# Kernel optimization log

Measured on AMD Instinct MI355X. Metric: run time of the kernel, lower is better.

## Reference

```python
import jax, jax.numpy as jnp
import numpy as np

# dims: S=seq_len, E=nenv, H=max_human_num, D=human_embedding_size, A=attention_size, NH=heads
S, E, H, D, A, NH = 128, 256, 20, 64, 64, 8
NEG = -1e9


def setup_inputs() -> dict:
    key = jax.random.key(0)
    ks = jax.random.split(key, 9)
    sc = 1.0 / np.sqrt(D).astype(np.float32)
    return {
        "h_temporal": jax.random.normal(ks[0], (S, E, 1, D), jnp.float32),
        "h_spatials": jax.random.normal(ks[1], (S, E, H, D), jnp.float32),
        "each_seq_len": jax.random.randint(ks[2], (S * E,), 0, H, dtype=jnp.int32),
        # per-head Linear params, stored [in, out] (equivalent to torch y = x W^T + b)
        "Wt": jax.random.normal(ks[3], (NH, D, A), jnp.float32) * sc,
        "bt": jax.random.normal(ks[4], (NH, A), jnp.float32) * 0.01,
        "Ws": jax.random.normal(ks[5], (NH, D, A), jnp.float32) * sc,
        "bs": jax.random.normal(ks[6], (NH, A), jnp.float32) * 0.01,
        # final merge linear: concat over heads (NH*D) -> D
        "Wf": jax.random.normal(ks[7], (NH * D, D), jnp.float32) / np.sqrt(NH * D).astype(np.float32),
        "bf": jax.random.normal(ks[8], (D,), jnp.float32) * 0.01,
    }


def reference(h_temporal, h_spatials, each_seq_len, Wt, bt, Ws, bs, Wf, bf):
    s, e, h, d = h_spatials.shape
    a = Wt.shape[-1]
    nh = Wt.shape[0]

    # per-head embeddings (heads vectorized instead of python loop)
    # temporal: [s,e,1,d] -> [s,e,nh,a] (the size-1 edge dim is summed out == squeeze)
    te = jnp.einsum('seoh,nha->sena', h_temporal, Wt) + bt            # [s,e,nh,a]
    sp = jnp.einsum('semh,nha->senma', h_spatials, Ws) + bs[:, None]  # [s,e,nh,h,a]

    # elementwise-product scoring, summed over attention dim, scaled by num_edges/sqrt(A)
    temperature = h / np.sqrt(a).astype(np.float32)
    scores = jnp.einsum('sena,senma->senm', te, sp) * temperature     # [s,e,nh,h]

    # mask: True for neighbor index j < each_seq_len (cumsum-of-onehot trick, closed form)
    mask = (jnp.arange(h)[None, :] < each_seq_len[:, None]).reshape(s, e, h)
    scores = jnp.where(mask[:, :, None, :], scores, NEG)
    attn = jax.nn.softmax(scores, axis=-1)                            # [s,e,nh,h]

    # weighted sum of spatial hidden states (the tiny bmm), per head
    wv = jnp.einsum('senm,semh->senh', attn, h_spatials)              # [s,e,nh,d]

    # concat heads (head-major, matching torch.cat over last dim) + final merge linear
    out = wv.reshape(s, e, 1, nh * d) @ Wf + bf                       # [s,e,1,d]
    return out
```

## Files before the change

### kernel.cpp

```cpp
#include <hip/hip_runtime.h>
#include <hip/hip_bf16.h>

typedef __attribute__((ext_vector_type(8))) short short8;
typedef __attribute__((ext_vector_type(4))) float f32x4;

constexpr float TEMP = 2.5f;
constexpr float NEGV = -1e9f;

constexpr int K_OFF  = 0;
constexpr int P_OFF  = 512;
constexpr int Q_OFF  = 1024;
constexpr int PFRAG  = 1040;
constexpr int MFRAG  = 2064;
constexpr int WFRAG  = 34832;

constexpr int HS2_U   = 0;
constexpr int HS2_PL  = 11520;
constexpr int V2_U    = 23040;
constexpr int V2_PL   = 4672;
constexpr int HT2_U   = 32384;
constexpr int ATT_F = 16832;
constexpr int C_F   = 18752;
constexpr int LEN_F = 18816;
constexpr int LDS_FL = 18824;

#define MFMA_B16 __builtin_amdgcn_mfma_f32_16x16x32_bf16

__device__ inline ushort bf16_rne(float x) {
  uint u = __float_as_uint(x);
  u += 0x7FFF + ((u >> 16) & 1);
  return (ushort)(u >> 16);
}
__device__ inline float bf16_f(ushort h) { return __uint_as_float(((uint)h) << 16); }
__device__ inline void split2(float x, ushort& h0, ushort& h1) {
  h0 = bf16_rne(x);
  h1 = bf16_rne(x - bf16_f(h0));
}
__device__ inline ushort split_lvl2(float x, int s) {
  ushort h0 = bf16_rne(x);
  return s == 0 ? h0 : bf16_rne(x - bf16_f(h0));
}
__device__ inline uint2 pkbf16x4(float4 v) {
  __hip_bfloat162 h0 = __float22bfloat162_rn(make_float2(v.x, v.y));
  __hip_bfloat162 h1 = __float22bfloat162_rn(make_float2(v.z, v.w));
  uint2 r; __builtin_memcpy(&r.x, &h0, 4); __builtin_memcpy(&r.y, &h1, 4);
  return r;
}
__device__ inline void pksplit4(float4 v, uint2& u0, uint2& u1) {
  u0 = pkbf16x4(v);
  float4 r;
  r.x = v.x - __uint_as_float(u0.x << 16);
  r.y = v.y - __uint_as_float(u0.x & 0xffff0000u);
  r.z = v.z - __uint_as_float(u0.y << 16);
  r.w = v.w - __uint_as_float(u0.y & 0xffff0000u);
  u1 = pkbf16x4(r);
}

__global__ __launch_bounds__(256) void prep_kernel(
    const float* __restrict__ Wt, const float* __restrict__ bt,
    const float* __restrict__ Ws, const float* __restrict__ bs,
    const float* __restrict__ Wf, float* __restrict__ ws) {
  __shared__ float AL[64 * 65];
  __shared__ float BL[64 * 65];
  __shared__ float ML[64 * 65];
  const int t = threadIdx.x;
  uint* wsu = (uint*)ws;
  if (blockIdx.x < 8) {
    const int n = blockIdx.x;
#pragma unroll
    for (int i = 0; i < 16; ++i) {
      int idx = i * 256 + t;
      AL[(idx >> 6) * 65 + (idx & 63)] = Wt[n * 4096 + idx];
      BL[(idx >> 6) * 65 + (idx & 63)] = Ws[n * 4096 + idx];
    }
    __syncthreads();
#pragma unroll
    for (int i = 0; i < 16; ++i) {
      int idx = i * 256 + t;
      int dp = idx >> 6, d = idx & 63;
      float acc = 0.f;
#pragma unroll 8
      for (int a = 0; a < 64; ++a) acc += AL[dp * 65 + a] * BL[d * 65 + a];
      ML[dp * 65 + d] = acc * TEMP;
    }
    if (t < 64) {
      float acc = 0.f;
#pragma unroll 8
      for (int a = 0; a < 64; ++a) acc += BL[t * 65 + a] * bt[n * 64 + a];
      ws[K_OFF + n * 64 + t] = acc * TEMP;
    } else if (t < 128) {
      int r = t - 64;
      float acc = 0.f;
#pragma unroll 8
      for (int a = 0; a < 64; ++a) acc += AL[r * 65 + a] * bs[n * 64 + a];
      ws[P_OFF + n * 64 + r] = acc * TEMP;
    } else if (t == 128) {
      float acc = 0.f;
      for (int a = 0; a < 64; ++a) acc += bt[n * 64 + a] * bs[n * 64 + a];
      ws[Q_OFF + n] = acc * TEMP;
    }
    __syncthreads();
#pragma unroll
    for (int i = 0; i < 16; ++i) {
      int f = i * 256 + t;
      int r = f & 3, lane = (f >> 2) & 63, g = f >> 8;
      int s = g & 1, dt = (g >> 1) & 3, ks = g >> 3;
      int k = ks * 32 + ((lane >> 4) & 3) * 8 + r * 2;
      int d = dt * 16 + (lane & 15);
      uint lo = split_lvl2(ML[k * 65 + d], s);
      uint hi = split_lvl2(ML[(k + 1) * 65 + d], s);
      wsu[MFRAG + n * 4096 + (((ks * 4 + dt) * 2 + s) * 64 + lane) * 4 + r] =
          lo | (hi << 16);
    }
  } else if (blockIdx.x < 16) {
    const int n = blockIdx.x - 8;
#pragma unroll
    for (int i = 0; i < 16; ++i) {
      int idx = i * 256 + t;
      AL[(idx >> 6) * 65 + (idx & 63)] = Wf[(n * 64 + (idx >> 6)) * 64 + (idx & 63)];
    }
    __syncthreads();
#pragma unroll
    for (int i = 0; i < 16; ++i) {
      int f = i * 256 + t;
      int r = f & 3, lane = (f >> 2) & 63, g = f >> 8;
      int s = g & 1, dt = (g >> 1) & 3, ks = g >> 3;
      int k = ks * 32 + ((lane >> 4) & 3) * 8 + r * 2;
      int d = dt * 16 + (lane & 15);
      uint lo = split_lvl2(AL[k * 65 + d], s);
      uint hi = split_lvl2(AL[(k + 1) * 65 + d], s);
      wsu[WFRAG + n * 4096 + (((ks * 4 + dt) * 2 + s) * 64 + lane) * 4 + r] =
          lo | (hi << 16);
    }
  } else {
#pragma unroll
    for (int i = 0; i < 2; ++i) {
      int idx = i * 256 + t;
      int n = idx >> 6, dp = idx & 63;
      float acc = 0.f;
#pragma unroll 8
      for (int a = 0; a < 64; ++a)
        acc += Wt[n * 4096 + dp * 64 + a] * bs[n * 64 + a];
      AL[idx] = acc * TEMP;
    }
    __syncthreads();
#pragma unroll
    for (int i = 0; i < 4; ++i) {
      int f = i * 256 + t;
      int r = f & 3, lane = (f >> 2) & 63, g = f >> 8;
      int s = g & 1, ks = g >> 1;
      int k = ks * 32 + ((lane >> 4) & 3) * 8 + r * 2;
      int col = lane & 15;
      uint lo = (col < 8) ? (uint)split_lvl2(AL[col * 64 + k], s) : 0u;
      uint hi = (col < 8) ? (uint)split_lvl2(AL[col * 64 + k + 1], s) : 0u;
      wsu[PFRAG + ((ks * 2 + s) * 64 + lane) * 4 + r] = lo | (hi << 16);
    }
  }
}

#define SPLIT2_MFMA(FB, DT, CC)                                      \
  {                                                                  \
    short8 b00 = *(const short8*)&(FB)[((0 * 4 + (DT)) * 2 + 0) * 256]; \
    short8 b01 = *(const short8*)&(FB)[((0 * 4 + (DT)) * 2 + 1) * 256]; \
    short8 b10 = *(const short8*)&(FB)[((1 * 4 + (DT)) * 2 + 0) * 256]; \
    short8 b11 = *(const short8*)&(FB)[((1 * 4 + (DT)) * 2 + 1) * 256]; \
    CC = MFMA_B16(a00, b00, CC, 0, 0, 0);                            \
    CC = MFMA_B16(a10, b10, CC, 0, 0, 0);                            \
    CC = MFMA_B16(a00, b01, CC, 0, 0, 0);                            \
    CC = MFMA_B16(a01, b00, CC, 0, 0, 0);                            \
    CC = MFMA_B16(a10, b11, CC, 0, 0, 0);                            \
    CC = MFMA_B16(a11, b10, CC, 0, 0, 0);                            \
  }

#define LOAD_A(BASEU, ROWSTR, PLANESTR, ROW, KOFF)                   \
  short8 a00 = *(const short8*)&(BASEU)[(ROW) * (ROWSTR) + (KOFF)];               \
  short8 a01 = *(const short8*)&(BASEU)[(PLANESTR) + (ROW) * (ROWSTR) + (KOFF)];  \
  short8 a10 = *(const short8*)&(BASEU)[(ROW) * (ROWSTR) + 32 + (KOFF)];          \
  short8 a11 = *(const short8*)&(BASEU)[(PLANESTR) + (ROW) * (ROWSTR) + 32 + (KOFF)];

#define HV_LOAD(I, DST)                                                      \
  {                                                                          \
    const int f_ = (I) * 512 + t;                                            \
    const int p_ = f_ / 320;                                                 \
    const int s_ = f_ - p_ * 320;                                            \
    DST = *(const float4*)(hs_g + (size_t)(pair0 + p_) * 1280 +              \
                           (s_ >> 4) * 64 + (s_ & 15) * 4);                  \
  }
#define HV_STORE(I, SRC)                                                     \
  {                                                                          \
    const int f_ = (I) * 512 + t;                                            \
    const int p_ = f_ / 320;                                                 \
    const int s_ = f_ - p_ * 320;                                            \
    uint2 u0_, u1_; pksplit4(SRC, u0_, u1_);                                 \
    ushort* d_ = ldsu + HS2_U + p_ * 1440 + (s_ >> 4) * 72 + (s_ & 15) * 4;  \
    *(uint2*)d_ = u0_;                                                       \
    *(uint2*)(d_ + HS2_PL) = u1_;                                            \
  }

__global__ __launch_bounds__(512, 4) void attn_kernel(
    const float* __restrict__ ht_g, const float* __restrict__ hs_g,
    const int* __restrict__ len_g, const float* __restrict__ bf,
    const float* __restrict__ wsp, float* __restrict__ out) {
  __shared__ __align__(16) float lds[LDS_FL];
  ushort* ldsu = (ushort*)lds;
  const int t    = threadIdx.x;
  const int lane = t & 63;
  const int w    = t >> 6;
  const int pair0 = blockIdx.x * 8;
  const uint* wsu = (const uint*)wsp;

  {
    float x = ht_g[(size_t)pair0 * 64 + t];
    ushort h0, h1; split2(x, h0, h1);
    const int p = t >> 6, dp = t & 63;
    ldsu[HT2_U + 0 * 640 + p * 80 + dp] = h0;
    ldsu[HT2_U + 1 * 640 + p * 80 + dp] = h1;
  }
  if (t < 8) lds[LEN_F + t] = (float)len_g[pair0 + t];
  __syncthreads();

  const int lo4 = lane & 15, kg = lane >> 4;
  const int rp8 = lo4 & 7;

  {
    const int n = w;
    LOAD_A(ldsu + HT2_U, 80, 640, rp8, kg * 8)
    const uint* fb = wsu + MFRAG + n * 4096 + lane * 4;
    const float* kb = &wsp[K_OFF + n * 64 + lo4];
    float kv0 = kb[0], kv1 = kb[16], kv2 = kb[32], kv3 = kb[48];
    f32x4 c0 = {kv0, kv0, kv0, kv0};
    f32x4 c1 = {kv1, kv1, kv1, kv1};
    f32x4 c2 = {kv2, kv2, kv2, kv2};
    f32x4 c3 = {kv3, kv3, kv3, kv3};
    SPLIT2_MFMA(fb, 0, c0)
    SPLIT2_MFMA(fb, 1, c1)
    SPLIT2_MFMA(fb, 2, c2)
    SPLIT2_MFMA(fb, 3, c3)
    if (kg < 2) {
#pragma unroll
      for (int reg = 0; reg < 4; ++reg) {
        const int p = kg * 4 + reg;
        ushort* vp = ldsu + V2_U + p * 584 + n * 72 + lo4;
        ushort h0, h1;
        split2(c0[reg], h0, h1); vp[0]  = h0; vp[V2_PL]      = h1;
        split2(c1[reg], h0, h1); vp[16] = h0; vp[V2_PL + 16] = h1;
        split2(c2[reg], h0, h1); vp[32] = h0; vp[V2_PL + 32] = h1;
        split2(c3[reg], h0, h1); vp[48] = h0; vp[V2_PL + 48] = h1;
      }
    }
  }

  float4 hv0, hv1, hv2, hv3, hv4;
  HV_LOAD(0, hv0) HV_LOAD(1, hv1) HV_LOAD(2, hv2) HV_LOAD(3, hv3) HV_LOAD(4, hv4)

  if (w == 0) {
    LOAD_A(ldsu + HT2_U, 80, 640, rp8, kg * 8)
    const uint* fbp = wsu + PFRAG + lane * 4;
    short8 b00 = *(const short8*)&fbp[0 * 256];
    short8 b01 = *(const short8*)&fbp[1 * 256];
    short8 b10 = *(const short8*)&fbp[2 * 256];
    short8 b11 = *(const short8*)&fbp[3 * 256];
    float qv = (lo4 < 8) ? wsp[Q_OFF + lo4] : 0.f;
    f32x4 cc = {qv, qv, qv, qv};
    cc = MFMA_B16(a00, b00, cc, 0, 0, 0);
    cc = MFMA_B16(a10, b10, cc, 0, 0, 0);
    cc = MFMA_B16(a00, b01, cc, 0, 0, 0);
    cc = MFMA_B16(a01, b00, cc, 0, 0, 0);
    cc = MFMA_B16(a10, b11, cc, 0, 0, 0);
    cc = MFMA_B16(a11, b10, cc, 0, 0, 0);
    if (kg < 2 && lo4 < 8) {
#pragma unroll
      for (int reg = 0; reg < 4; ++reg)
        lds[C_F + (kg * 4 + reg) * 8 + lo4] = cc[reg];
    }
  }

  HV_STORE(0, hv0) HV_STORE(1, hv1) HV_STORE(2, hv2) HV_STORE(3, hv3) HV_STORE(4, hv4)
  __syncthreads();

  {
    const int p = w;
    const int n8 = rp8;
    const int lenp = (int)lds[LEN_F + p];
    const ushort* vb = ldsu + V2_U + p * 584 + n8 * 72;
    const short8 B00 = *(const short8*)&vb[kg * 8];
    const short8 B01 = *(const short8*)&vb[V2_PL + kg * 8];
    const short8 B10 = *(const short8*)&vb[32 + kg * 8];
    const short8 B11 = *(const short8*)&vb[V2_PL + 32 + kg * 8];
    const float cv = lds[C_F + p * 8 + n8];
    f32x4 acc0 = {cv, cv, cv, cv};
    f32x4 acc1 = {cv, cv, cv, cv};
    {
      const ushort* ab = ldsu + HS2_U + p * 1440;
      LOAD_A(ab, 72, HS2_PL, lo4, kg * 8)
      acc0 = MFMA_B16(a00, B00, acc0, 0, 0, 0);
      acc0 = MFMA_B16(a10, B10, acc0, 0, 0, 0);
      acc0 = MFMA_B16(a00, B01, acc0, 0, 0, 0);
      acc0 = MFMA_B16(a01, B00, acc0, 0, 0, 0);
      acc0 = MFMA_B16(a10, B11, acc0, 0, 0, 0);
      acc0 = MFMA_B16(a11, B10, acc0, 0, 0, 0);
    }
    {
      const int row = (16 + lo4 < 20) ? (16 + lo4) : 19;
      const ushort* ab = ldsu + HS2_U + p * 1440;
      LOAD_A(ab, 72, HS2_PL, row, kg * 8)
      acc1 = MFMA_B16(a00, B00, acc1, 0, 0, 0);
      acc1 = MFMA_B16(a10, B10, acc1, 0, 0, 0);
      acc1 = MFMA_B16(a00, B01, acc1, 0, 0, 0);
      acc1 = MFMA_B16(a01, B00, acc1, 0, 0, 0);
      acc1 = MFMA_B16(a10, B11, acc1, 0, 0, 0);
      acc1 = MFMA_B16(a11, B10, acc1, 0, 0, 0);
    }
    float e0[4], e1[4];
    float mx = NEGV;
#pragma unroll
    for (int r = 0; r < 4; ++r) {
      const int m0 = kg * 4 + r;
      const int m1 = 16 + kg * 4 + r;
      e0[r] = (m0 < lenp) ? acc0[r] : NEGV;
      e1[r] = (m1 < lenp) ? acc1[r] : NEGV;
      mx = fmaxf(mx, fmaxf(e0[r], e1[r]));
    }
    mx = fmaxf(mx, __shfl_xor(mx, 16));
    mx = fmaxf(mx, __shfl_xor(mx, 32));
    float sm = 0.f;
#pragma unroll
    for (int r = 0; r < 4; ++r) {
      e0[r] = __expf(e0[r] - mx);
      e1[r] = (kg == 0) ? __expf(e1[r] - mx) : 0.f;
      sm += e0[r] + e1[r];
    }
    sm += __shfl_xor(sm, 16);
    sm += __shfl_xor(sm, 32);
    const float inv = 1.0f / sm;
    if (lo4 < 8) {
#pragma unroll
      for (int r = 0; r < 4; ++r)
        lds[ATT_F + p * 240 + (kg * 4 + r) * 12 + lo4] = e0[r] * inv;
      if (kg == 0) {
#pragma unroll
        for (int r = 0; r < 4; ++r)
          lds[ATT_F + p * 240 + (16 + r) * 12 + lo4] = e1[r] * inv;
      }
    }
  }

  {
    const int p = w, d = lane;
    const ushort* hsb = ldsu + HS2_U + p * 1440;
    float wv[8] = {0.f, 0.f, 0.f, 0.f, 0.f, 0.f, 0.f, 0.f};
    const float* atp = &lds[ATT_F + p * 240];
#pragma unroll
    for (int m_ = 0; m_ < 20; ++m_) {
      const float h = bf16_f(hsb[m_ * 72 + d]);
      const float4 a0 = *(const float4*)&atp[m_ * 12];
      const float4 a1 = *(const float4*)&atp[m_ * 12 + 4];
      wv[0] += a0.x * h; wv[1] += a0.y * h; wv[2] += a0.z * h; wv[3] += a0.w * h;
      wv[4] += a1.x * h; wv[5] += a1.y * h; wv[6] += a1.z * h; wv[7] += a1.w * h;
    }
    ushort* wp = ldsu + V2_U + p * 584;
#pragma unroll
    for (int n = 0; n < 8; ++n) {
      ushort h0, h1; split2(wv[n], h0, h1);
      wp[n * 72 + d] = h0;
      wp[V2_PL + n * 72 + d] = h1;
    }
  }
  __syncthreads();

  {
    const int dt = w & 3, ng = w >> 2;
    f32x4 cc = {0.f, 0.f, 0.f, 0.f};
#pragma unroll
    for (int nn = 0; nn < 4; ++nn) {
      const int n = ng * 4 + nn;
      LOAD_A(ldsu + V2_U, 584, V2_PL, rp8, n * 72 + kg * 8)
      const uint* fb = wsu + WFRAG + n * 4096 + lane * 4;
      SPLIT2_MFMA(fb, dt, cc)
    }
    if (kg < 2) {
#pragma unroll
      for (int reg = 0; reg < 4; ++reg)
        lds[0 + ng * 512 + (kg * 4 + reg) * 64 + dt * 16 + lo4] = cc[reg];
    }
  }
  __syncthreads();

  {
    const int d = t & 63;
    out[(size_t)pair0 * 64 + t] = bf[d] + lds[t] + lds[512 + t];
  }
}

extern "C" void kernel_launch(void* const* d_in, const int* in_sizes, int n_in,
                              void* d_out, int out_size, void* d_ws, size_t ws_size,
                              hipStream_t stream) {
  const float* ht  = (const float*)d_in[0];
  const float* hs  = (const float*)d_in[1];
  const int*   len = (const int*)d_in[2];
  const float* Wt  = (const float*)d_in[3];
  const float* bt  = (const float*)d_in[4];
  const float* Ws  = (const float*)d_in[5];
  const float* bs  = (const float*)d_in[6];
  const float* Wf  = (const float*)d_in[7];
  const float* bf  = (const float*)d_in[8];
  float* outp = (float*)d_out;
  float* ws   = (float*)d_ws;

  hipLaunchKernelGGL(prep_kernel, dim3(17), dim3(256), 0, stream,
                     Wt, bt, Ws, bs, Wf, ws);
  hipLaunchKernelGGL(attn_kernel, dim3(4096), dim3(512), 0, stream,
                     ht, hs, len, bf, ws, outp);
}
```

Baseline: 94.50 us.

## Use MFMA for attention-weighted sum and single-bf16 Wf with preloaded fragments

Replaces the scalar FMA loop for the per-head weighted sum of spatial states with bf16 MFMA ops, rounding attention weights to bf16. Drops the two-level bf16 split of Wf to a single bf16 plane, halving its workspace footprint and MFMA count in the merge stage. The Wf fragments are also loaded into registers at kernel start so their latency overlaps the earlier stages. This reduces precision in two places and raises register pressure, which may affect occupancy.

```diff
diff --git a/kernel.cpp b/kernel.cpp
--- a/kernel.cpp
+++ b/kernel.cpp
@@ -54,6 +54,11 @@
   r.z = v.z - __uint_as_float(u0.y << 16);
   r.w = v.w - __uint_as_float(u0.y & 0xffff0000u);
   u1 = pkbf16x4(r);
+}
+__device__ inline short8 pack4(uint a, uint b, uint c, uint d) {
+  union { uint u[4]; short8 s; } cv;
+  cv.u[0] = a; cv.u[1] = b; cv.u[2] = c; cv.u[3] = d;
+  return cv.s;
 }
 
 __global__ __launch_bounds__(256) void prep_kernel(
@@ -121,15 +126,15 @@
     }
     __syncthreads();
 #pragma unroll
-    for (int i = 0; i < 16; ++i) {
+    for (int i = 0; i < 8; ++i) {
       int f = i * 256 + t;
       int r = f & 3, lane = (f >> 2) & 63, g = f >> 8;
-      int s = g & 1, dt = (g >> 1) & 3, ks = g >> 3;
+      int dt = g & 3, ks = g >> 2;
       int k = ks * 32 + ((lane >> 4) & 3) * 8 + r * 2;
       int d = dt * 16 + (lane & 15);
-      uint lo = split_lvl2(AL[k * 65 + d], s);
-      uint hi = split_lvl2(AL[(k + 1) * 65 + d], s);
-      wsu[WFRAG + n * 4096 + (((ks * 4 + dt) * 2 + s) * 64 + lane) * 4 + r] =
+      uint lo = bf16_rne(AL[k * 65 + d]);
+      uint hi = bf16_rne(AL[(k + 1) * 65 + d]);
+      wsu[WFRAG + n * 2048 + ((ks * 4 + dt) * 64 + lane) * 4 + r] =
           lo | (hi << 16);
     }
   } else {
@@ -208,6 +213,17 @@
   const int w    = t >> 6;
   const int pair0 = blockIdx.x * 8;
   const uint* wsu = (const uint*)wsp;
+  const int lo4 = lane & 15, kg = lane >> 4;
+  const int rp8 = lo4 & 7;
+  const int dtw = w & 3, ngw = w >> 2;
+
+  short8 wfB0[4], wfB1[4];
+#pragma unroll
+  for (int nn = 0; nn < 4; ++nn) {
+    const uint* fb = wsu + WFRAG + (ngw * 4 + nn) * 2048 + lane * 4;
+    wfB0[nn] = *(const short8*)&fb[(0 * 4 + dtw) * 256];
+    wfB1[nn] = *(const short8*)&fb[(1 * 4 + dtw) * 256];
+  }
 
   {
     float x = ht_g[(size_t)pair0 * 64 + t];
@@ -218,9 +234,6 @@
   }
   if (t < 8) lds[LEN_F + t] = (float)len_g[pair0 + t];
   __syncthreads();
-
-  const int lo4 = lane & 15, kg = lane >> 4;
-  const int rp8 = lo4 & 7;
 
   {
     const int n = w;
@@ -346,42 +359,62 @@
   }
 
   {
-    const int p = w, d = lane;
+    const int p = w;
+    const float* atp = &lds[ATT_F + p * 240];
     const ushort* hsb = ldsu + HS2_U + p * 1440;
-    float wv[8] = {0.f, 0.f, 0.f, 0.f, 0.f, 0.f, 0.f, 0.f};
-    const float* atp = &lds[ATT_F + p * 240];
-#pragma unroll
-    for (int m_ = 0; m_ < 20; ++m_) {
-      const float h = bf16_f(hsb[m_ * 72 + d]);
-      const float4 a0 = *(const float4*)&atp[m_ * 12];
-      const float4 a1 = *(const float4*)&atp[m_ * 12 + 4];
-      wv[0] += a0.x * h; wv[1] += a0.y * h; wv[2] += a0.z * h; wv[3] += a0.w * h;
-      wv[4] += a1.x * h; wv[5] += a1.y * h; wv[6] += a1.z * h; wv[7] += a1.w * h;
-    }
+    uint a_[4];
+#pragma unroll
+    for (int r = 0; r < 4; ++r) {
+      const int m0 = kg * 8 + 2 * r;
+      float v0 = (m0 < 20) ? atp[m0 * 12 + lo4] : 0.f;
+      float v1 = (m0 + 1 < 20) ? atp[(m0 + 1) * 12 + lo4] : 0.f;
+      __hip_bfloat162 hh = __float22bfloat162_rn(make_float2(v0, v1));
+      __builtin_memcpy(&a_[r], &hh, 4);
+    }
+    const short8 A = pack4(a_[0], a_[1], a_[2], a_[3]);
     ushort* wp = ldsu + V2_U + p * 584;
 #pragma unroll
-    for (int n = 0; n < 8; ++n) {
-      ushort h0, h1; split2(wv[n], h0, h1);
-      wp[n * 72 + d] = h0;
-      wp[V2_PL + n * 72 + d] = h1;
+    for (int dt = 0; dt < 4; ++dt) {
+      uint b_[4];
+#pragma unroll
+      for (int r = 0; r < 4; ++r) {
+        const int m0 = kg * 8 + 2 * r;
+        const int d = dt * 16 + lo4;
+        uint blo = (m0 < 20) ? (uint)hsb[m0 * 72 + d] : 0u;
+        uint bhi = (m0 + 1 < 20) ? (uint)hsb[(m0 + 1) * 72 + d] : 0u;
+        b_[r] = blo | (bhi << 16);
+      }
+      const short8 B = pack4(b_[0], b_[1], b_[2], b_[3]);
+      f32x4 cc = {0.f, 0.f, 0.f, 0.f};
+      cc = MFMA_B16(A, B, cc, 0, 0, 0);
+      if (kg < 2) {
+#pragma unroll
+        for (int reg = 0; reg < 4; ++reg) {
+          const int n = kg * 4 + reg;
+          ushort h0, h1; split2(cc[reg], h0, h1);
+          wp[n * 72 + dt * 16 + lo4] = h0;
+          wp[V2_PL + n * 72 + dt * 16 + lo4] = h1;
+        }
+      }
     }
   }
   __syncthreads();
 
   {
-    const int dt = w & 3, ng = w >> 2;
     f32x4 cc = {0.f, 0.f, 0.f, 0.f};
 #pragma unroll
     for (int nn = 0; nn < 4; ++nn) {
-      const int n = ng * 4 + nn;
+      const int n = ngw * 4 + nn;
       LOAD_A(ldsu + V2_U, 584, V2_PL, rp8, n * 72 + kg * 8)
-      const uint* fb = wsu + WFRAG + n * 4096 + lane * 4;
-      SPLIT2_MFMA(fb, dt, cc)
+      cc = MFMA_B16(a00, wfB0[nn], cc, 0, 0, 0);
+      cc = MFMA_B16(a10, wfB1[nn], cc, 0, 0, 0);
+      cc = MFMA_B16(a01, wfB0[nn], cc, 0, 0, 0);
+      cc = MFMA_B16(a11, wfB1[nn], cc, 0, 0, 0);
     }
     if (kg < 2) {
 #pragma unroll
       for (int reg = 0; reg < 4; ++reg)
-        lds[0 + ng * 512 + (kg * 4 + reg) * 64 + dt * 16 + lo4] = cc[reg];
+        lds[0 + ngw * 512 + (kg * 4 + reg) * 64 + dtw * 16 + lo4] = cc[reg];
     }
   }
   __syncthreads();
```

After: 95.51 us. Within noise of the previous version (+1.1%).
